# Kernel tuning notes

Hardware: AMD Instinct MI355X
Metric: run time of the kernel (lower is better)

Reference implementation:

```python
import jax, jax.numpy as jnp
import numpy as np

DT = 1e-3   # timestep (s)
DH = 10.0   # grid spacing (m)


def setup_inputs() -> dict:
    key = jax.random.key(0)
    k1, k2, k3, k4 = jax.random.split(key, 4)
    B, NT, NZ, NX, NREC = 8, 256, 256, 256, 64
    x = jax.random.normal(k1, (B, NT), dtype=jnp.float32)            # source wavelets
    vp = 1500.0 + 2000.0 * jax.random.uniform(k2, (NZ, NX), dtype=jnp.float32)
    src_loc = jax.random.randint(k3, (B, 2), 4, NZ - 4, dtype=jnp.int32)        # (z,x) per shot
    rec_loc = jax.random.randint(k4, (B, NREC, 2), 4, NZ - 4, dtype=jnp.int32)  # (z,x) per rec
    return {"x": x, "vp": vp, "src_loc": src_loc, "rec_loc": rec_loc}


def reference(x, vp, src_loc, rec_loc):
    """Acoustic 2nd-order leapfrog FD time-stepping (WaveRNN pattern):
    per step: stencil update -> source scatter-inject -> receiver gather.
    Returns receiver traces (B, NT, NREC)."""
    B, NT = x.shape
    nz, nx = vp.shape
    c2dt2 = (vp * vp) * jnp.float32(DT * DT)   # (nz, nx), broadcast over batch
    inv_dh2 = jnp.float32(1.0 / (DH * DH))
    bidx = jnp.arange(B)
    sz, sx = src_loc[:, 0], src_loc[:, 1]
    rz, rx = rec_loc[..., 0], rec_loc[..., 1]

    def laplacian(h):  # 5-point stencil, zero (Dirichlet) boundaries
        interior = (h[:, 2:, 1:-1] + h[:, :-2, 1:-1]
                    + h[:, 1:-1, 2:] + h[:, 1:-1, :-2]
                    - 4.0 * h[:, 1:-1, 1:-1]) * inv_dh2
        return jnp.zeros_like(h).at[:, 1:-1, 1:-1].set(interior)

    def step(carry, wav_t):
        h1, h2 = carry                              # fields at t, t-1
        hn = 2.0 * h1 - h2 + c2dt2 * laplacian(h1)  # leapfrog update
        hn = hn.at[bidx, sz, sx].add(jnp.float32(DT * DT) * wav_t)  # source inject
        rec = hn[bidx[:, None], rz, rx]             # receiver gather (B, NREC)
        return (hn, h1), rec

    h0 = jnp.zeros((B, nz, nx), dtype=x.dtype)
    _, recs = jax.lax.scan(step, (h0, h0), x.T)     # recs: (NT, B, NREC)
    return jnp.transpose(recs, (1, 0, 2))           # (B, NT, NREC)
```

## Files before the change

### kernel.cpp

```cpp
#include <hip/hip_runtime.h>

typedef float v4f __attribute__((ext_vector_type(4)));

namespace {
constexpr int B_     = 8;
constexpr int NT_    = 256;
constexpr int NX_    = 256;
constexpr int NREC_  = 64;
constexpr int PIECES = 8;
constexpr int IROWS  = 32;
constexpr int G      = 16;
constexpr int ROUNDS = NT_ / G;
constexpr float DT2  = 1e-6f;
constexpr float KLAP = 1e-8f;
constexpr size_t FLAGS_BYTES = 4096;
constexpr int RCAP = 6;
}

__device__ __forceinline__ float dpp_shr1(float v) {
    return __int_as_float(__builtin_amdgcn_update_dpp(
        0, __float_as_int(v), 0x138 , 0xF, 0xF, true));
}
__device__ __forceinline__ float dpp_shl1(float v) {
    return __int_as_float(__builtin_amdgcn_update_dpp(
        0, __float_as_int(v), 0x130 , 0xF, 0xF, true));
}

__device__ __forceinline__ void store_v4_sys(float* p, v4f v) {
    asm volatile("global_store_dwordx4 %0, %1, off sc0 sc1"
                 :: "v"(p), "v"(v) : "memory");
}
__device__ __forceinline__ v4f load_v4_sys(const float* p) {
    v4f r;
    asm volatile("global_load_dwordx4 %0, %1, off sc0 sc1"
                 : "=v"(r) : "v"(p) : "memory");
    return r;
}

extern "C" __global__
__attribute__((amdgpu_flat_work_group_size(1024, 1024), amdgpu_waves_per_eu(4, 4)))
void wave_reg_kernel(const float* __restrict__ x,
                     const float* __restrict__ vp,
                     const int* __restrict__ src_loc,
                     const int* __restrict__ rec_loc,
                     float* __restrict__ out,
                     int* __restrict__ flags,
                     float* __restrict__ gbuf)
{
    __shared__ float pub[2][2][16][256];
    __shared__ float wav[NT_];
    __shared__ float recbuf[G][NREC_];
    __shared__ unsigned char recown[NREC_];

    const int bid  = blockIdx.x;
    const int b    = bid & 7;
    const int p    = bid >> 3;
    const int blk  = b * PIECES + p;
    const int tid  = threadIdx.x;
    const int band = tid >> 6;
    const int lane = tid & 63;
    const int c0   = lane << 2;
    const int grt  = p * IROWS - G + (band << 2);

    if (tid < NT_) wav[tid] = x[b * NT_ + tid];
    if (tid < NREC_) {
        int rz = rec_loc[(b * NREC_ + tid) * 2 + 0];
        recown[tid] = (rz >= p * IROWS && rz < p * IROWS + IROWS) ? 1 : 0;
    }

    v4f cf[4], cf2[4];
#pragma unroll
    for (int i = 0; i < 4; ++i) {
        int gr = grt + i;
        int crow = gr < 0 ? 0 : (gr > 255 ? 255 : gr);
        bool rowok = (gr >= 1) && (gr <= 254);
        v4f vv = *(const v4f*)&vp[crow * NX_ + c0];
        float cc[4];
#pragma unroll
        for (int k = 0; k < 4; ++k) {
            int col = c0 + k;
            float vk = (k == 0) ? vv.x : (k == 1) ? vv.y : (k == 2) ? vv.z : vv.w;
            cc[k] = (rowok && col >= 1 && col <= 254) ? vk * vk * KLAP : 0.f;
        }
        cf[i].x = cc[0]; cf[i].y = cc[1]; cf[i].z = cc[2]; cf[i].w = cc[3];
        cf2[i].x = 2.f - 4.f * cc[0]; cf2[i].y = 2.f - 4.f * cc[1];
        cf2[i].z = 2.f - 4.f * cc[2]; cf2[i].w = 2.f - 4.f * cc[3];
    }

    const int sz = src_loc[b * 2 + 0], sx = src_loc[b * 2 + 1];
    const int si = sz - grt;
    const int sj = sx - c0;
    const bool has_src = ((unsigned)si < 4u) && ((unsigned)sj < 4u);

    int rs[RCAP]; int rcnt = 0;
#pragma unroll 1
    for (int r = 0; r < NREC_; ++r) {
        int rz = rec_loc[(b * NREC_ + r) * 2 + 0];
        int rx = rec_loc[(b * NREC_ + r) * 2 + 1];
        int i = rz - grt, j = rx - c0;
        if (rz >= p * IROWS && rz < p * IROWS + IROWS &&
            (unsigned)i < 4u && (unsigned)j < 4u) {
            if (rcnt < RCAP) rs[rcnt] = (r << 4) | (i << 2) | j;
            ++rcnt;
        }
    }
    if (rcnt > RCAP) rcnt = RCAP;
    float* outb = out + (size_t)b * NT_ * NREC_;

    v4f A[4], Bv[4];
    {
        v4f z = {0.f, 0.f, 0.f, 0.f};
#pragma unroll
        for (int i = 0; i < 4; ++i) { A[i] = z; Bv[i] = z; }
    }

    auto gptr = [&](int e, int bk, int side, int lvl, int rr) -> float* {
        return gbuf + (((((size_t)(e & 1) * 64 + bk) * 2 + side) * 2 + lvl)
                       * 16 + rr) * 256;
    };

    auto step = [&](v4f (&C)[4], v4f (&P)[4], int t, int par) {
        *(v4f*)&pub[par][0][band][c0] = C[0];
        *(v4f*)&pub[par][1][band][c0] = C[3];
        __syncthreads();
        v4f nn, ss;
        if (band > 0)  nn = *(const v4f*)&pub[par][1][band - 1][c0];
        else           { nn.x = 0.f; nn.y = 0.f; nn.z = 0.f; nn.w = 0.f; }
        if (band < 15) ss = *(const v4f*)&pub[par][0][band + 1][c0];
        else           { ss.x = 0.f; ss.y = 0.f; ss.z = 0.f; ss.w = 0.f; }
        const float sv = DT2 * wav[t];
#pragma unroll
        for (int i = 0; i < 4; ++i) {
            v4f n = (i == 0) ? nn : C[i - 1];
            v4f s = (i == 3) ? ss : C[i + 1];
            float wv = dpp_shr1(C[i].w);
            float ev = dpp_shl1(C[i].x);
            v4f hn;
            { float sm = (n.x + s.x) + (wv     + C[i].y);
              hn.x = fmaf(cf[i].x, sm, fmaf(cf2[i].x, C[i].x, -P[i].x)); }
            { float sm = (n.y + s.y) + (C[i].x + C[i].z);
              hn.y = fmaf(cf[i].y, sm, fmaf(cf2[i].y, C[i].y, -P[i].y)); }
            { float sm = (n.z + s.z) + (C[i].y + C[i].w);
              hn.z = fmaf(cf[i].z, sm, fmaf(cf2[i].z, C[i].z, -P[i].z)); }
            { float sm = (n.w + s.w) + (C[i].z + ev);
              hn.w = fmaf(cf[i].w, sm, fmaf(cf2[i].w, C[i].w, -P[i].w)); }
            if (has_src && si == i) {
                if      (sj == 0) hn.x += sv;
                else if (sj == 1) hn.y += sv;
                else if (sj == 2) hn.z += sv;
                else              hn.w += sv;
            }
            P[i] = hn;
        }
#pragma unroll
        for (int k = 0; k < RCAP; ++k) {
            if (rcnt > k) {
                int pk = rs[k];
                int i = (pk >> 2) & 3, j = pk & 3, r = pk >> 4;
                v4f t01 = (i & 1) ? P[1] : P[0];
                v4f t23 = (i & 1) ? P[3] : P[2];
                v4f rw  = (i & 2) ? t23 : t01;
                float c01 = (j & 1) ? rw.y : rw.x;
                float c23 = (j & 1) ? rw.w : rw.z;
                recbuf[t & (G - 1)][r] = (j & 2) ? c23 : c01;
            }
        }
    };

    auto publish_prev = [&](int e) {
        if (band >= 4 && band < 12) {
            int side = (band >= 8) ? 1 : 0;
            int rr0 = (band << 2) - (side ? 32 : 16);
#pragma unroll
            for (int i = 0; i < 4; ++i)
                store_v4_sys(&gptr(e, blk, side, 1, rr0 + i)[c0], Bv[i]);
        }
    };

    auto exchange = [&](int e) {
        if (band >= 4 && band < 12) {
            int side = (band >= 8) ? 1 : 0;
            int rr0 = (band << 2) - (side ? 32 : 16);
#pragma unroll
            for (int i = 0; i < 4; ++i)
                store_v4_sys(&gptr(e, blk, side, 0, rr0 + i)[c0], A[i]);
        }
        __syncthreads();
        if (tid == 0)
            __hip_atomic_store(&flags[blk], e + 1, __ATOMIC_RELAXED,
                               __HIP_MEMORY_SCOPE_SYSTEM);
        if (band < 4 && p > 0) {
            if (lane == 0)
                while (__hip_atomic_load(&flags[blk - 1], __ATOMIC_RELAXED,
                                         __HIP_MEMORY_SCOPE_SYSTEM) < e + 1)
                    __builtin_amdgcn_s_sleep(1);
            int rr0 = band << 2;
#pragma unroll
            for (int i = 0; i < 4; ++i) {
                A[i]  = load_v4_sys(&gptr(e, blk - 1, 1, 0, rr0 + i)[c0]);
                Bv[i] = load_v4_sys(&gptr(e, blk - 1, 1, 1, rr0 + i)[c0]);
            }
        }
        if (band >= 12 && p < PIECES - 1) {
            if (lane == 0)
                while (__hip_atomic_load(&flags[blk + 1], __ATOMIC_RELAXED,
                                         __HIP_MEMORY_SCOPE_SYSTEM) < e + 1)
                    __builtin_amdgcn_s_sleep(1);
            int rr0 = (band << 2) - 48;
#pragma unroll
            for (int i = 0; i < 4; ++i) {
                A[i]  = load_v4_sys(&gptr(e, blk + 1, 0, 0, rr0 + i)[c0]);
                Bv[i] = load_v4_sys(&gptr(e, blk + 1, 0, 1, rr0 + i)[c0]);
            }
        }
        asm volatile("s_waitcnt vmcnt(0)" ::: "memory");
        __builtin_amdgcn_sched_barrier(0);
        __syncthreads();
    };

    int t = 0;
#pragma unroll 1
    for (int e = 0; e < ROUNDS; ++e) {
#pragma unroll 1
        for (int s = 0; s < G; s += 2) {
            step(A, Bv, t, 0);
            if (s == G - 2 && e < ROUNDS - 1)
                publish_prev(e);
            step(Bv, A, t + 1, 1);
            t += 2;
        }
        __syncthreads();
        {
            int s = tid >> 6;
            int r = tid & 63;
            if (recown[r]) outb[(e * G + s) * NREC_ + r] = recbuf[s][r];
        }
        if (e < ROUNDS - 1) exchange(e);
    }
}

extern "C" void kernel_launch(void* const* d_in, const int* in_sizes, int n_in,
                              void* d_out, int out_size, void* d_ws, size_t ws_size,
                              hipStream_t stream) {
    const float* x   = (const float*)d_in[0];
    const float* vp  = (const float*)d_in[1];
    const int*   src = (const int*)d_in[2];
    const int*   rec = (const int*)d_in[3];
    float*       o   = (float*)d_out;
    int*   flags = (int*)d_ws;
    float* gbuf  = (float*)((char*)d_ws + FLAGS_BYTES);
    (void)hipMemsetAsync(d_ws, 0, FLAGS_BYTES, stream);
    hipLaunchKernelGGL(wave_reg_kernel, dim3(B_ * PIECES), dim3(1024), 0, stream,
                       x, vp, src, rec, o, flags, gbuf);
}
```

Measured before the change: 346.7 us.

## Split domain into 16 pieces per shot with smaller blocks and wave-uniform src/rec skips

```diff
diff --git a/kernel.cpp b/kernel.cpp
--- a/kernel.cpp
+++ b/kernel.cpp
@@ -7,10 +7,13 @@
 constexpr int NT_    = 256;
 constexpr int NX_    = 256;
 constexpr int NREC_  = 64;
-constexpr int PIECES = 8;
-constexpr int IROWS  = 32;
+constexpr int PIECES = 16;
+constexpr int IROWS  = 16;
 constexpr int G      = 16;
 constexpr int ROUNDS = NT_ / G;
+constexpr int NB     = (IROWS + 2 * G) / 4;
+constexpr int NTHR   = NB * 64;
+constexpr int NBLK   = B_ * PIECES;
 constexpr float DT2  = 1e-6f;
 constexpr float KLAP = 1e-8f;
 constexpr size_t FLAGS_BYTES = 4096;
@@ -38,7 +41,7 @@
 }
 
 extern "C" __global__
-__attribute__((amdgpu_flat_work_group_size(1024, 1024), amdgpu_waves_per_eu(4, 4)))
+__attribute__((amdgpu_flat_work_group_size(NTHR, NTHR), amdgpu_waves_per_eu(4, 4)))
 void wave_reg_kernel(const float* __restrict__ x,
                      const float* __restrict__ vp,
                      const int* __restrict__ src_loc,
@@ -47,7 +50,7 @@
                      int* __restrict__ flags,
                      float* __restrict__ gbuf)
 {
-    __shared__ float pub[2][2][16][256];
+    __shared__ float pub[2][2][NB][256];
     __shared__ float wav[NT_];
     __shared__ float recbuf[G][NREC_];
     __shared__ unsigned char recown[NREC_];
@@ -91,6 +94,7 @@
     const int si = sz - grt;
     const int sj = sx - c0;
     const bool has_src = ((unsigned)si < 4u) && ((unsigned)sj < 4u);
+    const bool wave_has_src = __any(has_src);
 
     int rs[RCAP]; int rcnt = 0;
 #pragma unroll 1
@@ -105,6 +109,7 @@
         }
     }
     if (rcnt > RCAP) rcnt = RCAP;
+    const bool wave_has_rec = __any(rcnt > 0);
     float* outb = out + (size_t)b * NT_ * NREC_;
 
     v4f A[4], Bv[4];
@@ -114,9 +119,8 @@
         for (int i = 0; i < 4; ++i) { A[i] = z; Bv[i] = z; }
     }
 
-    auto gptr = [&](int e, int bk, int side, int lvl, int rr) -> float* {
-        return gbuf + (((((size_t)(e & 1) * 64 + bk) * 2 + side) * 2 + lvl)
-                       * 16 + rr) * 256;
+    auto gptr = [&](int e, int bk, int lvl, int rr) -> float* {
+        return gbuf + ((((size_t)(e & 1) * NBLK + bk) * 2 + lvl) * 16 + rr) * 256;
     };
 
     auto step = [&](v4f (&C)[4], v4f (&P)[4], int t, int par) {
@@ -124,11 +128,10 @@
         *(v4f*)&pub[par][1][band][c0] = C[3];
         __syncthreads();
         v4f nn, ss;
-        if (band > 0)  nn = *(const v4f*)&pub[par][1][band - 1][c0];
-        else           { nn.x = 0.f; nn.y = 0.f; nn.z = 0.f; nn.w = 0.f; }
-        if (band < 15) ss = *(const v4f*)&pub[par][0][band + 1][c0];
-        else           { ss.x = 0.f; ss.y = 0.f; ss.z = 0.f; ss.w = 0.f; }
-        const float sv = DT2 * wav[t];
+        if (band > 0)      nn = *(const v4f*)&pub[par][1][band - 1][c0];
+        else               { nn.x = 0.f; nn.y = 0.f; nn.z = 0.f; nn.w = 0.f; }
+        if (band < NB - 1) ss = *(const v4f*)&pub[par][0][band + 1][c0];
+        else               { ss.x = 0.f; ss.y = 0.f; ss.z = 0.f; ss.w = 0.f; }
 #pragma unroll
         for (int i = 0; i < 4; ++i) {
             v4f n = (i == 0) ? nn : C[i - 1];
@@ -144,46 +147,52 @@
               hn.z = fmaf(cf[i].z, sm, fmaf(cf2[i].z, C[i].z, -P[i].z)); }
             { float sm = (n.w + s.w) + (C[i].z + ev);
               hn.w = fmaf(cf[i].w, sm, fmaf(cf2[i].w, C[i].w, -P[i].w)); }
-            if (has_src && si == i) {
-                if      (sj == 0) hn.x += sv;
-                else if (sj == 1) hn.y += sv;
-                else if (sj == 2) hn.z += sv;
-                else              hn.w += sv;
-            }
             P[i] = hn;
         }
-#pragma unroll
-        for (int k = 0; k < RCAP; ++k) {
-            if (rcnt > k) {
-                int pk = rs[k];
-                int i = (pk >> 2) & 3, j = pk & 3, r = pk >> 4;
-                v4f t01 = (i & 1) ? P[1] : P[0];
-                v4f t23 = (i & 1) ? P[3] : P[2];
-                v4f rw  = (i & 2) ? t23 : t01;
-                float c01 = (j & 1) ? rw.y : rw.x;
-                float c23 = (j & 1) ? rw.w : rw.z;
-                recbuf[t & (G - 1)][r] = (j & 2) ? c23 : c01;
+        if (wave_has_src) {
+            const float sv = DT2 * wav[t];
+#pragma unroll
+            for (int i = 0; i < 4; ++i) {
+                if (has_src && si == i) {
+                    if      (sj == 0) P[i].x += sv;
+                    else if (sj == 1) P[i].y += sv;
+                    else if (sj == 2) P[i].z += sv;
+                    else              P[i].w += sv;
+                }
+            }
+        }
+        if (wave_has_rec) {
+#pragma unroll
+            for (int k = 0; k < RCAP; ++k) {
+                if (rcnt > k) {
+                    int pk = rs[k];
+                    int i = (pk >> 2) & 3, j = pk & 3, r = pk >> 4;
+                    v4f t01 = (i & 1) ? P[1] : P[0];
+                    v4f t23 = (i & 1) ? P[3] : P[2];
+                    v4f rw  = (i & 2) ? t23 : t01;
+                    float c01 = (j & 1) ? rw.y : rw.x;
+                    float c23 = (j & 1) ? rw.w : rw.z;
+                    recbuf[t & (G - 1)][r] = (j & 2) ? c23 : c01;
+                }
             }
         }
     };
 
     auto publish_prev = [&](int e) {
-        if (band >= 4 && band < 12) {
-            int side = (band >= 8) ? 1 : 0;
-            int rr0 = (band << 2) - (side ? 32 : 16);
+        if (band >= 4 && band < 8) {
+            int rr0 = (band - 4) << 2;
 #pragma unroll
             for (int i = 0; i < 4; ++i)
-                store_v4_sys(&gptr(e, blk, side, 1, rr0 + i)[c0], Bv[i]);
+                store_v4_sys(&gptr(e, blk, 1, rr0 + i)[c0], Bv[i]);
         }
     };
 
     auto exchange = [&](int e) {
-        if (band >= 4 && band < 12) {
-            int side = (band >= 8) ? 1 : 0;
-            int rr0 = (band << 2) - (side ? 32 : 16);
+        if (band >= 4 && band < 8) {
+            int rr0 = (band - 4) << 2;
 #pragma unroll
             for (int i = 0; i < 4; ++i)
-                store_v4_sys(&gptr(e, blk, side, 0, rr0 + i)[c0], A[i]);
+                store_v4_sys(&gptr(e, blk, 0, rr0 + i)[c0], A[i]);
         }
         __syncthreads();
         if (tid == 0)
@@ -197,20 +206,20 @@
             int rr0 = band << 2;
 #pragma unroll
             for (int i = 0; i < 4; ++i) {
-                A[i]  = load_v4_sys(&gptr(e, blk - 1, 1, 0, rr0 + i)[c0]);
-                Bv[i] = load_v4_sys(&gptr(e, blk - 1, 1, 1, rr0 + i)[c0]);
-            }
-        }
-        if (band >= 12 && p < PIECES - 1) {
+                A[i]  = load_v4_sys(&gptr(e, blk - 1, 0, rr0 + i)[c0]);
+                Bv[i] = load_v4_sys(&gptr(e, blk - 1, 1, rr0 + i)[c0]);
+            }
+        }
+        if (band >= 8 && p < PIECES - 1) {
             if (lane == 0)
                 while (__hip_atomic_load(&flags[blk + 1], __ATOMIC_RELAXED,
                                          __HIP_MEMORY_SCOPE_SYSTEM) < e + 1)
                     __builtin_amdgcn_s_sleep(1);
-            int rr0 = (band << 2) - 48;
+            int rr0 = (band - 8) << 2;
 #pragma unroll
             for (int i = 0; i < 4; ++i) {
-                A[i]  = load_v4_sys(&gptr(e, blk + 1, 0, 0, rr0 + i)[c0]);
-                Bv[i] = load_v4_sys(&gptr(e, blk + 1, 0, 1, rr0 + i)[c0]);
+                A[i]  = load_v4_sys(&gptr(e, blk + 1, 0, rr0 + i)[c0]);
+                Bv[i] = load_v4_sys(&gptr(e, blk + 1, 1, rr0 + i)[c0]);
             }
         }
         asm volatile("s_waitcnt vmcnt(0)" ::: "memory");
@@ -230,9 +239,9 @@
             t += 2;
         }
         __syncthreads();
-        {
-            int s = tid >> 6;
-            int r = tid & 63;
+#pragma unroll 1
+        for (int idx = tid; idx < G * NREC_; idx += NTHR) {
+            int s = idx >> 6, r = idx & 63;
             if (recown[r]) outb[(e * G + s) * NREC_ + r] = recbuf[s][r];
         }
         if (e < ROUNDS - 1) exchange(e);
@@ -250,6 +259,6 @@
     int*   flags = (int*)d_ws;
     float* gbuf  = (float*)((char*)d_ws + FLAGS_BYTES);
     (void)hipMemsetAsync(d_ws, 0, FLAGS_BYTES, stream);
-    hipLaunchKernelGGL(wave_reg_kernel, dim3(B_ * PIECES), dim3(1024), 0, stream,
+    hipLaunchKernelGGL(wave_reg_kernel, dim3(NBLK), dim3(NTHR), 0, stream,
                        x, vp, src, rec, o, flags, gbuf);
 }
```

New measurement: 296.3 us. -14.6%, faster.
